# Kernel optimization log

Measured on AMD Instinct MI355X. Metric: run time of the kernel, lower is better.

Reference implementation:

```python
import jax, jax.numpy as jnp
import numpy as np

APP_DIM = 27
FEA_PE = 6
VIEW_PE = 6
FEATURE_C = 128
DENSITY_SHIFT = -10.0
DISTANCE_SCALE = 25.0
IN_MLPC = 2 * VIEW_PE * 3 + 2 * FEA_PE * APP_DIM + 3 + APP_DIM  # 390


def positional_encoding(x, freqs):
    # x: [..., C] -> [..., 2*freqs*C]
    freq_bands = (2.0 ** jnp.arange(freqs)).astype(x.dtype)
    pts = (x[..., None] * freq_bands).reshape(x.shape[:-1] + (freqs * x.shape[-1],))
    return jnp.concatenate([jnp.sin(pts), jnp.cos(pts)], axis=-1)


def alpha2weights(alpha):
    # alpha: [N_rays, N_samples]; last sample forced opaque (as in source)
    alpha = alpha.at[:, -1].set(1.0)
    trans = jnp.concatenate(
        [jnp.ones((alpha.shape[0], 1), alpha.dtype), 1.0 - alpha + 1e-10], axis=-1)
    T = jnp.cumprod(trans, axis=-1)
    weights = alpha * T[:, :-1]
    return weights, T


def setup_inputs() -> dict:
    key = jax.random.key(0)
    ks = jax.random.split(key, 12)
    N_rays, N_samples = 4096, 128
    sigma_feat = jax.random.normal(ks[0], (N_rays, N_samples), jnp.float32)
    app_features = 0.1 * jax.random.normal(ks[1], (N_rays, N_samples, APP_DIM), jnp.float32)
    vd = jax.random.normal(ks[2], (N_rays, N_samples, 3), jnp.float32)
    viewdirs = vd / (jnp.linalg.norm(vd, axis=-1, keepdims=True) + 1e-8)
    dists = 0.02 * jax.random.uniform(ks[3], (N_rays, N_samples), jnp.float32)

    def linear(k, fan_in, fan_out):
        kw, kb = jax.random.split(k)
        lim = 1.0 / np.sqrt(fan_in)
        W = jax.random.uniform(kw, (fan_in, fan_out), jnp.float32, -lim, lim)
        b = jax.random.uniform(kb, (fan_out,), jnp.float32, -lim, lim)
        return W, b

    W1, b1 = linear(ks[4], IN_MLPC, FEATURE_C)
    W2, b2 = linear(ks[5], FEATURE_C, FEATURE_C)
    W3, _ = linear(ks[6], FEATURE_C, 3)
    b3 = jnp.zeros((3,), jnp.float32)  # bias of last layer initialized to 0 in source
    return {"sigma_feat": sigma_feat, "app_features": app_features,
            "viewdirs": viewdirs, "dists": dists,
            "W1": W1, "b1": b1, "W2": W2, "b2": b2, "W3": W3, "b3": b3}


def reference(sigma_feat, app_features, viewdirs, dists, W1, b1, W2, b2, W3, b3):
    # feature2density: softplus with density_shift
    sigma = jax.nn.softplus(sigma_feat + DENSITY_SHIFT)
    alpha = 1.0 - jnp.exp(-sigma * dists * DISTANCE_SCALE)  # [N_rays, N_samples]
    weights, _T = alpha2weights(alpha)

    # MLPRender_Fea: cat[features, viewdirs, PE(features), PE(viewdirs)]
    mlp_in = jnp.concatenate(
        [app_features, viewdirs,
         positional_encoding(app_features, FEA_PE),
         positional_encoding(viewdirs, VIEW_PE)], axis=-1)  # [R, S, 390]
    h = jax.nn.relu(jnp.einsum('rsc,cf->rsf', mlp_in, W1) + b1)
    h = jax.nn.relu(jnp.einsum('rsf,fg->rsg', h, W2) + b2)
    rgb = jax.nn.sigmoid(jnp.einsum('rsg,go->rso', h, W3) + b3)  # [R, S, 3]

    rgb_map = jnp.sum(weights[..., None] * rgb, axis=-2)  # [R, 3]
    return rgb_map
```

## Files before the change

kernel.cpp:

```cpp
#include <hip/hip_runtime.h>
#include <math.h>

typedef unsigned short u16;
using bf16x8 = __attribute__((ext_vector_type(8))) short;
using f32x4  = __attribute__((ext_vector_type(4))) float;

#define NS      128
#define RAYS_PER_BLOCK 2
#define NBLOCKS (4096 / RAYS_PER_BLOCK)
#define KS1     15
#define NSLICE  19

#define OW0   0
#define OW1   4096
#define OX0   8192
#define OX1   12288
#define OH1   8192
#define POOLSZ 24576

__device__ __forceinline__ u16 f2bf(float f) {
    unsigned int i = __float_as_uint(f);
    return (u16)((i + 0x7FFFu + ((i >> 16) & 1u)) >> 16);
}

__device__ __forceinline__ unsigned pk(float hi, float lo) {
    unsigned a = __float_as_uint(hi) + 0x8000u;
    unsigned b = __float_as_uint(lo) + 0x8000u;
    return __builtin_amdgcn_perm(a, b, 0x07060302u);
}
__device__ __forceinline__ u16 f2bf1(float f) {
    return (u16)((__float_as_uint(f) + 0x8000u) >> 16);
}

__device__ __forceinline__ int afoff(int m, int k) {
    return ((((k >> 5) * 8 + (m >> 4)) * 64) + (((k >> 3) & 3) * 16) + (m & 15)) * 8 + (k & 7);
}

__device__ __forceinline__ void stage_w(const u16* g, u16* l, int wave, int lane) {
    #pragma unroll
    for (int c = 0; c < 2; ++c) {
        const u16* gp = g + (wave * 2 + c) * 512 + lane * 8;
        u16* lp = l + (wave * 2 + c) * 512;
        __builtin_amdgcn_global_load_lds(
            (const __attribute__((address_space(1))) unsigned int*)gp,
            (__attribute__((address_space(3))) unsigned int*)lp, 16, 0, 0);
    }
}

__device__ __forceinline__ int orig_k(int ch, int slot) {
    if (ch < 27) {
        if (slot == 0) return ch;
        if (slot <= 6) return 30 + ch * 6 + (slot - 1);
        return 192 + ch * 6 + (slot - 7);
    } else {
        int c = ch - 27;
        if (slot == 0) return 27 + c;
        if (slot <= 6) return 354 + c * 6 + (slot - 1);
        return 372 + c * 6 + (slot - 7);
    }
}

__device__ __forceinline__ void build_x(u16* Xb, int m_b, int cl_b, float v) {
    float rev = v * 0.15915494309189535f;
    rev -= floorf(rev);
    float s0 = __builtin_amdgcn_sinf(rev);
    float c0 = __builtin_amdgcn_cosf(rev);
    float s1 = 2.f * s0 * c0, c1 = c0 * c0 - s0 * s0;
    float s2 = 2.f * s1 * c1, c2 = c1 * c1 - s1 * s1;
    float s3 = 2.f * s2 * c2, c3 = c2 * c2 - s2 * s2;
    float s4 = 2.f * s3 * c3, c4 = c3 * c3 - s3 * s3;
    float s5 = 2.f * s4 * c4, c5 = c4 * c4 - s4 * s4;
    uint4 lo, hi;
    lo.x = pk(s0, v);  lo.y = pk(s2, s1);  lo.z = pk(s4, s3);  lo.w = pk(c0, s5);
    hi.x = pk(c2, c1); hi.y = pk(c4, c3);  hi.z = pk(0.f, c5); hi.w = 0u;
    int base = (m_b >> 4) * 512 + ((2 * cl_b) * 16 + (m_b & 15)) * 8;
    *(uint4*)(Xb + base)       = lo;
    *(uint4*)(Xb + base + 128) = hi;
}

__global__ __launch_bounds__(256) void prep_kernel(
    const float* __restrict__ W1, const float* __restrict__ W2,
    const float* __restrict__ W3, u16* __restrict__ ws)
{
    int idx = blockIdx.x * 256 + threadIdx.x;
    if (idx < 61440) {
        int j = idx & 7, lane = (idx >> 3) & 63, nt = (idx >> 9) & 7, ks = idx >> 12;
        int q = lane >> 4, l15 = lane & 15;
        int klocal = q * 8 + j;
        int ch = ks * 2 + (klocal >> 4);
        int slot = klocal & 15;
        int n = nt * 16 + l15;
        ws[idx] = (slot < 13) ? f2bf(W1[orig_k(ch, slot) * 128 + n]) : (u16)0;
    } else if (idx < 77824) {
        int i2 = idx - 61440;
        int j = i2 & 7, lane = (i2 >> 3) & 63, nt = (i2 >> 9) & 7, ks = i2 >> 12;
        int k = ks * 32 + (lane >> 4) * 8 + j;
        int n = nt * 16 + (lane & 15);
        ws[idx] = f2bf(W2[k * 128 + n]);
    } else if (idx < 79872) {
        int i3 = idx - 77824;
        int j = i3 & 7, lane = (i3 >> 3) & 63, ks = i3 >> 9;
        int k = ks * 32 + (lane >> 4) * 8 + j;
        int n = lane & 15;
        ws[idx] = (n < 3) ? f2bf(W3[k * 3 + n]) : (u16)0;
    }
}

__global__ __launch_bounds__(256, 3) void render_kernel(
    const float* __restrict__ sigma_g, const float* __restrict__ app_g,
    const float* __restrict__ view_g,  const float* __restrict__ dists_g,
    const float* __restrict__ b1_g,    const float* __restrict__ b2_g,
    const float* __restrict__ b3_g,    const u16* __restrict__ ws,
    float* __restrict__ out_g)
{
    __shared__ __align__(16) u16 pool[POOLSZ];
    __shared__ float scanS;
    __shared__ float sum2[6];
    float* part = (float*)(pool + OW0);

    const int tid  = threadIdx.x;
    const int lane = tid & 63;
    const int wave = tid >> 6;
    const int l15  = lane & 15;
    const int quad = lane >> 4;
    const int wm   = wave >> 1;
    const int wn   = wave & 1;

    const u16* w3r = ws + 77824;

    float b1r[4], b2r[4];
    #pragma unroll
    for (int nt = 0; nt < 4; ++nt) {
        int col = wn * 64 + nt * 16 + l15;
        b1r[nt] = b1_g[col];
        b2r[nt] = b2_g[col];
    }
    const float b3v = (l15 < 3) ? b3_g[l15] : 0.f;
    bf16x8 w3fr[4];
    #pragma unroll
    for (int ks = 0; ks < 4; ++ks)
        w3fr[ks] = *(const bf16x8*)(w3r + (ks * 64 + lane) * 8);

    const int m_b  = tid >> 1;
    const int cl_b = tid & 1;

    #pragma unroll 1
    for (int ri = 0; ri < RAYS_PER_BLOCK; ++ri) {
        const int r  = blockIdx.x * RAYS_PER_BLOCK + ri;
        const int rb = r * NS;
        const float* ap = app_g  + (rb + m_b) * 27;
        const float* vp = view_g + (rb + m_b) * 3;

        float pv_cur = ap[cl_b];
        float pv_nxt = ap[2 + cl_b];

        stage_w(ws, pool + OW0, wave, lane);

        float alpha = 0.f, prod = 1.f, wr = 0.f;
        if (tid < NS) {
            float x  = sigma_g[rb + tid] - 10.f;
            float sp = (x > 20.f) ? x : log1pf(expf(x));
            alpha = 1.f - expf(-sp * dists_g[rb + tid] * 25.f);
            if (tid == NS - 1) alpha = 1.f;
            float tb = 1.f - alpha + 1e-10f;
            prod = tb;
            #pragma unroll
            for (int d = 1; d < 64; d <<= 1) {
                float v = __shfl_up(prod, d);
                if (lane >= d) prod *= v;
            }
            if (tid == 63) scanS = prod;
        }

        build_x(pool + OX0, m_b, cl_b, pv_cur);
        pv_cur = pv_nxt;
        __syncthreads();

        if (tid < NS) {
            float prev = __shfl_up(prod, 1);
            float base = (lane == 0) ? 1.f : prev;
            float scale = (wave == 1) ? scanS : 1.f;
            wr = alpha * base * scale;
        }

        const f32x4 vzero = {0.f, 0.f, 0.f, 0.f};
        f32x4 acc[4][4];
        #pragma unroll
        for (int mt = 0; mt < 4; ++mt)
            #pragma unroll
            for (int nt = 0; nt < 4; ++nt) acc[mt][nt] = vzero;

        #pragma unroll 1
        for (int i = 0; i < NSLICE; ++i) {
            if (i + 1 < NSLICE)
                stage_w(ws + (i + 1) * 4096,
                        pool + ((((i + 1) & 1) == 0) ? OW0 : OW1), wave, lane);
            if (i + 2 < KS1) {
                int ch = 2 * (i + 2) + cl_b;
                pv_nxt = (ch < 27) ? ap[ch] : vp[ch - 27];
            }

            const u16* Wb = pool + (((i & 1) == 0) ? OW0 : OW1);
            const u16* Asrc = (i < KS1)
                ? (pool + (((i & 1) == 0) ? OX0 : OX1))
                : (pool + OH1 + (i - KS1) * 4096);
            bf16x8 a[4];
            #pragma unroll
            for (int mt = 0; mt < 4; ++mt)
                a[mt] = *(const bf16x8*)(Asrc + ((wm * 4 + mt) * 64 + lane) * 8);
            #pragma unroll
            for (int nt = 0; nt < 4; ++nt) {
                bf16x8 b = *(const bf16x8*)(Wb + ((wn * 4 + nt) * 64 + lane) * 8);
                #pragma unroll
                for (int mt = 0; mt < 4; ++mt)
                    acc[mt][nt] = __builtin_amdgcn_mfma_f32_16x16x32_bf16(a[mt], b, acc[mt][nt], 0, 0, 0);
            }
            if (i < KS1 - 1) {
                u16* Xb = pool + ((((i + 1) & 1) == 0) ? OX0 : OX1);
                build_x(Xb, m_b, cl_b, pv_cur);
                pv_cur = pv_nxt;
            }
            if (i == KS1 - 1) {
                __syncthreads();
                #pragma unroll
                for (int mt = 0; mt < 4; ++mt)
                    #pragma unroll
                    for (int nt = 0; nt < 4; ++nt) {
                        int col = wn * 64 + nt * 16 + l15;
                        #pragma unroll
                        for (int rr = 0; rr < 4; ++rr) {
                            int row = wm * 64 + mt * 16 + quad * 4 + rr;
                            pool[OH1 + afoff(row, col)] =
                                f2bf1(fmaxf(acc[mt][nt][rr] + b1r[nt], 0.f));
                        }
                        acc[mt][nt] = vzero;
                    }
            }
            __syncthreads();
        }

        #pragma unroll
        for (int mt = 0; mt < 4; ++mt)
            #pragma unroll
            for (int nt = 0; nt < 4; ++nt) {
                int col = wn * 64 + nt * 16 + l15;
                #pragma unroll
                for (int rr = 0; rr < 4; ++rr) {
                    int row = wm * 64 + mt * 16 + quad * 4 + rr;
                    pool[OH1 + afoff(row, col)] =
                        f2bf1(fmaxf(acc[mt][nt][rr] + b2r[nt], 0.f));
                }
            }
        __syncthreads();

        f32x4 acc3[2] = {vzero, vzero};
        #pragma unroll
        for (int mi = 0; mi < 2; ++mi) {
            int mtt = wn * 2 + mi;
            #pragma unroll
            for (int ks = 0; ks < 4; ++ks) {
                bf16x8 a3 = *(const bf16x8*)(pool + OH1 + ks * 4096 +
                    ((wm * 4 + mtt) * 64 + lane) * 8);
                acc3[mi] = __builtin_amdgcn_mfma_f32_16x16x32_bf16(a3, w3fr[ks], acc3[mi], 0, 0, 0);
            }
        }
        if (l15 < 3) {
            #pragma unroll
            for (int mi = 0; mi < 2; ++mi) {
                int mtt = wn * 2 + mi;
                #pragma unroll
                for (int rr = 0; rr < 4; ++rr) {
                    int row = wm * 64 + mtt * 16 + quad * 4 + rr;
                    float v = acc3[mi][rr] + b3v;
                    part[row * 3 + l15] = 1.f / (1.f + expf(-v));
                }
            }
        }
        __syncthreads();

        float v0 = 0.f, v1 = 0.f, v2 = 0.f;
        if (tid < NS) {
            v0 = wr * part[tid * 3 + 0];
            v1 = wr * part[tid * 3 + 1];
            v2 = wr * part[tid * 3 + 2];
            #pragma unroll
            for (int d = 1; d < 64; d <<= 1) {
                v0 += __shfl_xor(v0, d);
                v1 += __shfl_xor(v1, d);
                v2 += __shfl_xor(v2, d);
            }
            if (lane == 0) {
                sum2[wave * 3 + 0] = v0;
                sum2[wave * 3 + 1] = v1;
                sum2[wave * 3 + 2] = v2;
            }
        }
        __syncthreads();
        if (tid == 0) {
            out_g[r * 3 + 0] = sum2[0] + sum2[3];
            out_g[r * 3 + 1] = sum2[1] + sum2[4];
            out_g[r * 3 + 2] = sum2[2] + sum2[5];
        }
        __syncthreads();
    }
}

extern "C" void kernel_launch(void* const* d_in, const int* in_sizes, int n_in,
                              void* d_out, int out_size, void* d_ws, size_t ws_size,
                              hipStream_t stream) {
    (void)in_sizes; (void)n_in; (void)out_size; (void)ws_size;
    const float* sigma = (const float*)d_in[0];
    const float* app   = (const float*)d_in[1];
    const float* view  = (const float*)d_in[2];
    const float* dists = (const float*)d_in[3];
    const float* W1    = (const float*)d_in[4];
    const float* b1    = (const float*)d_in[5];
    const float* W2    = (const float*)d_in[6];
    const float* b2    = (const float*)d_in[7];
    const float* W3    = (const float*)d_in[8];
    const float* b3    = (const float*)d_in[9];
    float* out = (float*)d_out;

    u16* ws = (u16*)d_ws;

    prep_kernel<<<312, 256, 0, stream>>>(W1, W2, W3, ws);
    render_kernel<<<NBLOCKS, 256, 0, stream>>>(sigma, app, view, dists,
                                               b1, b2, b3, ws, out);
}
```

Measured before the change: 217.8 us.

## Load weight fragments from global into registers instead of staging through LDS

Weight B-fragments are now loaded straight from global memory (L2-cached) into registers, with a one-slice register prefetch, instead of being staged into double-buffered LDS with global_load_lds. This shrinks LDS use, which could raise occupancy, and drops the per-slice barrier for slices that only read weights. The slice loop is fully unrolled. The hidden-activation writeback now packs pairs of bf16 values with lane shuffles into 32-bit LDS stores. The trade-off is higher register pressure and global-load latency sitting on the MFMA critical path.

```diff
diff --git a/kernel.cpp b/kernel.cpp
--- a/kernel.cpp
+++ b/kernel.cpp
@@ -2,6 +2,7 @@
 #include <math.h>
 
 typedef unsigned short u16;
+typedef unsigned int   u32;
 using bf16x8 = __attribute__((ext_vector_type(8))) short;
 using f32x4  = __attribute__((ext_vector_type(4))) float;
 
@@ -11,12 +12,9 @@
 #define KS1     15
 #define NSLICE  19
 
-#define OW0   0
-#define OW1   4096
-#define OX0   8192
-#define OX1   12288
-#define OH1   8192
-#define POOLSZ 24576
+#define OX0   0
+#define OX1   4096
+#define POOLSZ 16384
 
 __device__ __forceinline__ u16 f2bf(float f) {
     unsigned int i = __float_as_uint(f);
@@ -28,23 +26,9 @@
     unsigned b = __float_as_uint(lo) + 0x8000u;
     return __builtin_amdgcn_perm(a, b, 0x07060302u);
 }
-__device__ __forceinline__ u16 f2bf1(float f) {
-    return (u16)((__float_as_uint(f) + 0x8000u) >> 16);
-}
 
 __device__ __forceinline__ int afoff(int m, int k) {
     return ((((k >> 5) * 8 + (m >> 4)) * 64) + (((k >> 3) & 3) * 16) + (m & 15)) * 8 + (k & 7);
-}
-
-__device__ __forceinline__ void stage_w(const u16* g, u16* l, int wave, int lane) {
-    #pragma unroll
-    for (int c = 0; c < 2; ++c) {
-        const u16* gp = g + (wave * 2 + c) * 512 + lane * 8;
-        u16* lp = l + (wave * 2 + c) * 512;
-        __builtin_amdgcn_global_load_lds(
-            (const __attribute__((address_space(1))) unsigned int*)gp,
-            (__attribute__((address_space(3))) unsigned int*)lp, 16, 0, 0);
-    }
 }
 
 __device__ __forceinline__ int orig_k(int ch, int slot) {
@@ -114,9 +98,9 @@
     float* __restrict__ out_g)
 {
     __shared__ __align__(16) u16 pool[POOLSZ];
+    __shared__ float part[NS * 3];
     __shared__ float scanS;
     __shared__ float sum2[6];
-    float* part = (float*)(pool + OW0);
 
     const int tid  = threadIdx.x;
     const int lane = tid & 63;
@@ -125,8 +109,10 @@
     const int quad = lane >> 4;
     const int wm   = wave >> 1;
     const int wn   = wave & 1;
+    const bool odd = (l15 & 1);
 
     const u16* w3r = ws + 77824;
+    const int boff0 = ((wn * 4 + 0) * 64 + lane) * 8;
 
     float b1r[4], b2r[4];
     #pragma unroll
@@ -136,10 +122,6 @@
         b2r[nt] = b2_g[col];
     }
     const float b3v = (l15 < 3) ? b3_g[l15] : 0.f;
-    bf16x8 w3fr[4];
-    #pragma unroll
-    for (int ks = 0; ks < 4; ++ks)
-        w3fr[ks] = *(const bf16x8*)(w3r + (ks * 64 + lane) * 8);
 
     const int m_b  = tid >> 1;
     const int cl_b = tid & 1;
@@ -154,7 +136,10 @@
         float pv_cur = ap[cl_b];
         float pv_nxt = ap[2 + cl_b];
 
-        stage_w(ws, pool + OW0, wave, lane);
+        bf16x8 bc[4];
+        #pragma unroll
+        for (int nt = 0; nt < 4; ++nt)
+            bc[nt] = *(const bf16x8*)(ws + boff0 + nt * 512);
 
         float alpha = 0.f, prod = 1.f, wr = 0.f;
         if (tid < NS) {
@@ -190,66 +175,85 @@
             #pragma unroll
             for (int nt = 0; nt < 4; ++nt) acc[mt][nt] = vzero;
 
-        #pragma unroll 1
+        #pragma unroll
         for (int i = 0; i < NSLICE; ++i) {
-            if (i + 1 < NSLICE)
-                stage_w(ws + (i + 1) * 4096,
-                        pool + ((((i + 1) & 1) == 0) ? OW0 : OW1), wave, lane);
+            bf16x8 bn[4];
+            if (i + 1 < NSLICE) {
+                #pragma unroll
+                for (int nt = 0; nt < 4; ++nt)
+                    bn[nt] = *(const bf16x8*)(ws + (i + 1) * 4096 + boff0 + nt * 512);
+            }
             if (i + 2 < KS1) {
                 int ch = 2 * (i + 2) + cl_b;
                 pv_nxt = (ch < 27) ? ap[ch] : vp[ch - 27];
             }
 
-            const u16* Wb = pool + (((i & 1) == 0) ? OW0 : OW1);
             const u16* Asrc = (i < KS1)
                 ? (pool + (((i & 1) == 0) ? OX0 : OX1))
-                : (pool + OH1 + (i - KS1) * 4096);
+                : (pool + (i - KS1) * 4096);
             bf16x8 a[4];
             #pragma unroll
             for (int mt = 0; mt < 4; ++mt)
                 a[mt] = *(const bf16x8*)(Asrc + ((wm * 4 + mt) * 64 + lane) * 8);
             #pragma unroll
-            for (int nt = 0; nt < 4; ++nt) {
-                bf16x8 b = *(const bf16x8*)(Wb + ((wn * 4 + nt) * 64 + lane) * 8);
+            for (int nt = 0; nt < 4; ++nt)
                 #pragma unroll
                 for (int mt = 0; mt < 4; ++mt)
-                    acc[mt][nt] = __builtin_amdgcn_mfma_f32_16x16x32_bf16(a[mt], b, acc[mt][nt], 0, 0, 0);
-            }
+                    acc[mt][nt] = __builtin_amdgcn_mfma_f32_16x16x32_bf16(a[mt], bc[nt], acc[mt][nt], 0, 0, 0);
+
             if (i < KS1 - 1) {
                 u16* Xb = pool + ((((i + 1) & 1) == 0) ? OX0 : OX1);
                 build_x(Xb, m_b, cl_b, pv_cur);
                 pv_cur = pv_nxt;
-            }
-            if (i == KS1 - 1) {
+                __syncthreads();
+            } else if (i == KS1 - 1) {
                 __syncthreads();
                 #pragma unroll
                 for (int mt = 0; mt < 4; ++mt)
                     #pragma unroll
                     for (int nt = 0; nt < 4; ++nt) {
-                        int col = wn * 64 + nt * 16 + l15;
-                        #pragma unroll
-                        for (int rr = 0; rr < 4; ++rr) {
-                            int row = wm * 64 + mt * 16 + quad * 4 + rr;
-                            pool[OH1 + afoff(row, col)] =
-                                f2bf1(fmaxf(acc[mt][nt][rr] + b1r[nt], 0.f));
-                        }
+                        float u0 = fmaxf(acc[mt][nt][0] + b1r[nt], 0.f);
+                        float u1 = fmaxf(acc[mt][nt][1] + b1r[nt], 0.f);
+                        float u2 = fmaxf(acc[mt][nt][2] + b1r[nt], 0.f);
+                        float u3 = fmaxf(acc[mt][nt][3] + b1r[nt], 0.f);
+                        float r0 = __shfl_xor(odd ? u0 : u2, 1);
+                        float r1 = __shfl_xor(odd ? u1 : u3, 1);
+                        unsigned d0 = pk(odd ? u2 : r0, odd ? r0 : u0);
+                        unsigned d1 = pk(odd ? u3 : r1, odd ? r1 : u1);
+                        int row0 = wm * 64 + mt * 16 + quad * 4 + (odd ? 2 : 0);
+                        int colp = wn * 64 + nt * 16 + (l15 & ~1);
+                        *(u32*)(pool + afoff(row0, colp))     = d0;
+                        *(u32*)(pool + afoff(row0 + 1, colp)) = d1;
                         acc[mt][nt] = vzero;
                     }
-            }
-            __syncthreads();
-        }
-
+                __syncthreads();
+            }
+            #pragma unroll
+            for (int nt = 0; nt < 4; ++nt) bc[nt] = bn[nt];
+        }
+
+        bf16x8 w3fr[4];
+        #pragma unroll
+        for (int ks = 0; ks < 4; ++ks)
+            w3fr[ks] = *(const bf16x8*)(w3r + (ks * 64 + lane) * 8);
+
+        __syncthreads();
         #pragma unroll
         for (int mt = 0; mt < 4; ++mt)
             #pragma unroll
             for (int nt = 0; nt < 4; ++nt) {
-                int col = wn * 64 + nt * 16 + l15;
-                #pragma unroll
-                for (int rr = 0; rr < 4; ++rr) {
-                    int row = wm * 64 + mt * 16 + quad * 4 + rr;
-                    pool[OH1 + afoff(row, col)] =
-                        f2bf1(fmaxf(acc[mt][nt][rr] + b2r[nt], 0.f));
-                }
+                float u0 = fmaxf(acc[mt][nt][0] + b2r[nt], 0.f);
+                float u1 = fmaxf(acc[mt][nt][1] + b2r[nt], 0.f);
+                float u2 = fmaxf(acc[mt][nt][2] + b2r[nt], 0.f);
+                float u3 = fmaxf(acc[mt][nt][3] + b2r[nt], 0.f);
+                float r0 = __shfl_xor(odd ? u0 : u2, 1);
+                float r1 = __shfl_xor(odd ? u1 : u3, 1);
+                unsigned d0 = pk(odd ? u2 : r0, odd ? r0 : u0);
+                unsigned d1 = pk(odd ? u3 : r1, odd ? r1 : u1);
+                int row0 = wm * 64 + mt * 16 + quad * 4 + (odd ? 2 : 0);
+                int colp = wn * 64 + nt * 16 + (l15 & ~1);
+                *(u32*)(pool + afoff(row0, colp))     = d0;
+                *(u32*)(pool + afoff(row0 + 1, colp)) = d1;
             }
         __syncthreads();
 
@@ -259,7 +263,7 @@
             int mtt = wn * 2 + mi;
             #pragma unroll
             for (int ks = 0; ks < 4; ++ks) {
-                bf16x8 a3 = *(const bf16x8*)(pool + OH1 + ks * 4096 +
+                bf16x8 a3 = *(const bf16x8*)(pool + ks * 4096 +
                     ((wm * 4 + mtt) * 64 + lane) * 8);
                 acc3[mi] = __builtin_amdgcn_mfma_f32_16x16x32_bf16(a3, w3fr[ks], acc3[mi], 0, 0, 0);
             }
```

Result: slower. 614.6 us (+182.2%).
